# Kernel tuning notes

Measured on AMD Instinct MI355X. Metric: run time of the kernel, lower is better.

The kernel has to match this reference:

```python
import jax, jax.numpy as jnp
import numpy as np

N_HEADS = 8
ATT_DIM = 64


def _pos_enc(x):
    # x: (chan, L, bs, D); sinusoidal PE added along axis -3 (the query/key slot dim)
    L, D = x.shape[-3], x.shape[-1]
    pos = np.arange(L)[:, None].astype(np.float32)
    div = np.exp(np.arange(0, D, 2).astype(np.float32) * (-np.log(10000.0) / D))
    pe = np.zeros((L, 1, D), dtype=np.float32)
    pe[:, 0, 0::2] = np.sin(pos * div)
    pe[:, 0, 1::2] = np.cos(pos * div)
    return x + jnp.asarray(pe)


def setup_inputs() -> dict:
    key = jax.random.key(0)
    ks = jax.random.split(key, 6)
    C, NQ, NK, B, QD, KD = 8, 16, 32, 128, 128, 128
    E = N_HEADS * ATT_DIM  # 512
    OUT = ATT_DIM  # out_dim defaults to attention_dim
    b = np.float32(1.0 / np.sqrt(ATT_DIM))
    bp = np.float32(1.0 / np.sqrt(OUT))
    return {
        "q": jax.random.normal(ks[0], (C, NQ, B, QD), dtype=jnp.float32),
        "k": jax.random.normal(ks[1], (C, NK, B, KD), dtype=jnp.float32),
        "Wq": jax.random.uniform(ks[2], (C, NQ, QD, E), jnp.float32, -b, b),
        "Wk": jax.random.uniform(ks[3], (C, NK, KD, E), jnp.float32, -b, b),
        "Wv": jax.random.uniform(ks[4], (C, NK, KD, E), jnp.float32, -b, b),
        "Wp": jax.random.uniform(ks[5], (C, NQ, E, OUT), jnp.float32, -bp, bp),
    }


def reference(q, k, Wq, Wk, Wv, Wp):
    H, A = N_HEADS, ATT_DIM
    C, NQ, B, _ = q.shape
    NK = k.shape[1]
    inv_temp = jnp.float32(1.0 / np.sqrt(A))
    q_pe = _pos_enc(q)
    k_pe = _pos_enc(k)
    # per-channel grouped QKV projections: (C, N, B, D) x (C, N, D, E) -> (C, N, B, E)
    query = jnp.einsum('cqbd,cqde->cqbe', q_pe, Wq).reshape(C, NQ, B, H, A)
    key_t = jnp.einsum('ckbd,ckde->ckbe', k_pe, Wk).reshape(C, NK, B, H, A)
    value = jnp.einsum('ckbd,ckde->ckbe', k_pe, Wv).reshape(C, NK, B, H, A)
    # attention scores per (channel, batch, head)
    logits = jnp.einsum('cqbha,ckbha->cbhqk', query, key_t) * inv_temp
    attn = jax.nn.softmax(logits, axis=-1)
    # value aggregation (original does broadcast-multiply+sum; einsum is the same math)
    out = jnp.einsum('cbhqk,ckbha->cqbha', attn, value).reshape(C, NQ, B, H * A)
    # per-channel output projection
    return jnp.einsum('cqbe,cqeo->cqbo', out, Wp)
```

## Files before the change

kernel.cpp:

```cpp
#include <hip/hip_runtime.h>

#define C_  8
#define NQ_ 16
#define NK_ 32
#define B_  128
#define D_  128
#define E_  512
#define H_  8
#define A_  64
#define O_  64

typedef __attribute__((ext_vector_type(4))) float f32x4;
typedef __attribute__((ext_vector_type(8))) short bf16x8;
typedef __attribute__((ext_vector_type(4))) short bf16x4;

__device__ __forceinline__ short f2bf(float f) {
    union { float f; unsigned u; } v; v.f = f;
    unsigned r = v.u + 0x7fffu + ((v.u >> 16) & 1u);
    return (short)(r >> 16);
}

__global__ __launch_bounds__(256) void qkv_proj_kernel(
    const float* __restrict__ qin, const float* __restrict__ kin,
    const float* __restrict__ Wq, const float* __restrict__ Wk,
    const float* __restrict__ Wv,
    short* __restrict__ wsq, short* __restrict__ wsk, short* __restrict__ wsv)
{
    __shared__ __align__(16) short Alds[B_][72];
    __shared__ __align__(16) short Blds[128][72];
    __shared__ float pe_buf[D_];

    const int tid   = threadIdx.x;
    const int blk   = blockIdx.x;
    const int e_blk = blk & 3;
    const int unit  = blk >> 2;

    const float* X; const float* W; short* Y; int n;
    if (unit < C_ * NQ_) {
        n = unit % NQ_;
        X = qin + (size_t)unit * B_ * D_;
        W = Wq  + (size_t)unit * D_ * E_;
        Y = wsq + (size_t)unit * B_ * E_;
    } else if (unit < C_ * (NQ_ + NK_)) {
        const int u = unit - C_ * NQ_;
        n = u % NK_;
        X = kin + (size_t)u * B_ * D_;
        W = Wk  + (size_t)u * D_ * E_;
        Y = wsk + (size_t)u * B_ * E_;
    } else {
        const int u = unit - C_ * (NQ_ + NK_);
        n = u % NK_;
        X = kin + (size_t)u * B_ * D_;
        W = Wv  + (size_t)u * D_ * E_;
        Y = wsv + (size_t)u * B_ * E_;
    }

    if (tid < D_) {
        const int d = tid;
        const float freq = expf((float)(d & ~1) * (-9.210340371976184f / (float)D_));
        const float arg  = (float)n * freq;
        pe_buf[d] = (d & 1) ? cosf(arg) : sinf(arg);
    }
    __syncthreads();

    const int wv   = tid >> 6;
    const int lane = tid & 63;
    const int lr   = lane & 15;
    const int quad = lane >> 4;
    const int wrow = (wv >> 1) * 64;
    const int wcol = (wv & 1) * 64;

    f32x4 acc[4][4];
    for (int m = 0; m < 4; ++m)
        for (int nf = 0; nf < 4; ++nf)
            acc[m][nf] = (f32x4){0.f, 0.f, 0.f, 0.f};

    const int e  = tid & 127;
    const int kg = (tid >> 7) * 32;

    for (int k0 = 0; k0 < D_; k0 += 64) {
        f32x4 a_raw[8];
        #pragma unroll
        for (int i = 0; i < 8; ++i) {
            const int id  = tid + 256 * i;
            const int row = id >> 4;
            const int ch  = id & 15;
            a_raw[i] = *(const f32x4*)(X + (size_t)row * D_ + k0 + ch * 4);
        }
        float b_raw[32];
        const float* bsrc = W + (size_t)(k0 + kg) * E_ + e_blk * 128 + e;
        #pragma unroll
        for (int i = 0; i < 32; ++i)
            b_raw[i] = bsrc[(size_t)i * E_];

        #pragma unroll
        for (int i = 0; i < 8; ++i) {
            const int id  = tid + 256 * i;
            const int row = id >> 4;
            const int ch  = id & 15;
            bf16x4 v;
            #pragma unroll
            for (int j = 0; j < 4; ++j)
                v[j] = f2bf(a_raw[i][j] + pe_buf[k0 + ch * 4 + j]);
            *(bf16x4*)&Alds[row][ch * 4] = v;
        }
        #pragma unroll
        for (int i = 0; i < 4; ++i) {
            bf16x8 v;
            #pragma unroll
            for (int j = 0; j < 8; ++j)
                v[j] = f2bf(b_raw[i * 8 + j]);
            *(bf16x8*)&Blds[e][kg + i * 8] = v;
        }
        __syncthreads();

        for (int ks = 0; ks < 2; ++ks) {
            const int kc = ks * 32 + quad * 8;
            bf16x8 af[4], bfr[4];
            for (int m = 0; m < 4; ++m)
                af[m] = *(const bf16x8*)&Alds[wrow + m * 16 + lr][kc];
            for (int nf = 0; nf < 4; ++nf)
                bfr[nf] = *(const bf16x8*)&Blds[wcol + nf * 16 + lr][kc];
            for (int m = 0; m < 4; ++m)
                for (int nf = 0; nf < 4; ++nf)
                    acc[m][nf] = __builtin_amdgcn_mfma_f32_16x16x32_bf16(
                        af[m], bfr[nf], acc[m][nf], 0, 0, 0);
        }
        __syncthreads();
    }

    for (int m = 0; m < 4; ++m)
        for (int nf = 0; nf < 4; ++nf)
            for (int r = 0; r < 4; ++r) {
                const int row = wrow + m * 16 + quad * 4 + r;
                const int col = e_blk * 128 + wcol + nf * 16 + lr;
                Y[(size_t)row * E_ + col] = f2bf(acc[m][nf][r]);
            }
}

__global__ __launch_bounds__(256) void attn_kernel(
    const short* __restrict__ wsq, const short* __restrict__ wsk,
    const short* __restrict__ wsv, short* __restrict__ wso)
{
    __shared__ __align__(16) short Qs[16][264];
    __shared__ __align__(16) short Ks[32][264];
    __shared__ __align__(16) short Vs[32][258];
    __shared__ __align__(16) short Ps[4][16][40];

    const int tid = threadIdx.x;
    const int blk = blockIdx.x;
    const int hh  = blk & 1;
    const int b   = (blk >> 1) & (B_ - 1);
    const int c   = blk >> 8;

    const size_t rowstride = (size_t)B_ * E_;
    const size_t ebase = (size_t)b * E_ + hh * 256;

    {
        const int nloc = tid >> 5;
        const int bi   = tid & 31;
        const short* qb = wsq + (size_t)c * NQ_ * rowstride + ebase + bi * 8;
        const short* kb = wsk + (size_t)c * NK_ * rowstride + ebase + bi * 8;
        const short* vb = wsv + (size_t)c * NK_ * rowstride + ebase + bi * 8;
        #pragma unroll
        for (int i = 0; i < 2; ++i) {
            const int nn = nloc + i * 8;
            *(bf16x8*)&Qs[nn][bi * 8] = *(const bf16x8*)(qb + (size_t)nn * rowstride);
        }
        #pragma unroll
        for (int i = 0; i < 4; ++i) {
            const int nn = nloc + i * 8;
            *(bf16x8*)&Ks[nn][bi * 8] = *(const bf16x8*)(kb + (size_t)nn * rowstride);
        }
        #pragma unroll
        for (int i = 0; i < 4; ++i) {
            const int nn = nloc + i * 8;
            bf16x8 v = *(const bf16x8*)(vb + (size_t)nn * rowstride);
            #pragma unroll
            for (int p = 0; p < 4; ++p)
                *(int*)&Vs[nn][bi * 8 + p * 2] = ((const int*)&v)[p];
        }
    }
    __syncthreads();

    const int wv   = tid >> 6;
    const int lane = tid & 63;
    const int lr   = lane & 15;
    const int quad = lane >> 4;
    const int lcol = wv * 64;

    f32x4 sacc0 = (f32x4){0.f, 0.f, 0.f, 0.f};
    f32x4 sacc1 = (f32x4){0.f, 0.f, 0.f, 0.f};
    #pragma unroll
    for (int ks = 0; ks < 2; ++ks) {
        const int kc = lcol + ks * 32 + quad * 8;
        const bf16x8 aq  = *(const bf16x8*)&Qs[lr][kc];
        const bf16x8 bk0 = *(const bf16x8*)&Ks[lr][kc];
        const bf16x8 bk1 = *(const bf16x8*)&Ks[16 + lr][kc];
        sacc0 = __builtin_amdgcn_mfma_f32_16x16x32_bf16(aq, bk0, sacc0, 0, 0, 0);
        sacc1 = __builtin_amdgcn_mfma_f32_16x16x32_bf16(aq, bk1, sacc1, 0, 0, 0);
    }

    float p0[4], p1[4];
    for (int r = 0; r < 4; ++r) {
        const float v0 = sacc0[r] * 0.125f;
        const float v1 = sacc1[r] * 0.125f;
        float m = fmaxf(v0, v1);
        m = fmaxf(m, __shfl_xor(m, 1));
        m = fmaxf(m, __shfl_xor(m, 2));
        m = fmaxf(m, __shfl_xor(m, 4));
        m = fmaxf(m, __shfl_xor(m, 8));
        const float e0 = __expf(v0 - m);
        const float e1 = __expf(v1 - m);
        float s = e0 + e1;
        s += __shfl_xor(s, 1);
        s += __shfl_xor(s, 2);
        s += __shfl_xor(s, 4);
        s += __shfl_xor(s, 8);
        const float inv = 1.0f / s;
        p0[r] = e0 * inv;
        p1[r] = e1 * inv;
    }

    for (int r = 0; r < 4; ++r) {
        Ps[wv][quad * 4 + r][lr]      = f2bf(p0[r]);
        Ps[wv][quad * 4 + r][16 + lr] = f2bf(p1[r]);
    }
    __syncthreads();
    const bf16x8 ap = *(const bf16x8*)&Ps[wv][lr][quad * 8];

    #pragma unroll
    for (int t = 0; t < 4; ++t) {
        bf16x8 bvv;
        #pragma unroll
        for (int j = 0; j < 8; ++j)
            bvv[j] = Vs[quad * 8 + j][lcol + t * 16 + lr];
        f32x4 oacc = (f32x4){0.f, 0.f, 0.f, 0.f};
        oacc = __builtin_amdgcn_mfma_f32_16x16x32_bf16(ap, bvv, oacc, 0, 0, 0);
        for (int r = 0; r < 4; ++r)
            wso[((size_t)(c * NQ_ + quad * 4 + r) * B_ + b) * E_
                + hh * 256 + lcol + t * 16 + lr] = f2bf(oacc[r]);
    }
}

__global__ __launch_bounds__(256) void out_proj_kernel(
    const short* __restrict__ wso, const float* __restrict__ Wp,
    float* __restrict__ out)
{
    __shared__ __align__(16) short Xlds[64][72];
    __shared__ __align__(16) short Wlds[64][72];

    const int tid  = threadIdx.x;
    const int blk  = blockIdx.x;
    const int cq   = blk >> 1;
    const int half = blk & 1;

    const short* Xb = wso + (size_t)cq * B_ * E_ + (size_t)half * 64 * E_;
    const float* Wb = Wp  + (size_t)cq * E_ * O_;
    float*       Ob = out + (size_t)cq * B_ * O_ + (size_t)half * 64 * O_;

    const int wv   = tid >> 6;
    const int lane = tid & 63;
    const int lr   = lane & 15;
    const int quad = lane >> 4;

    f32x4 acc[4];
    for (int nf = 0; nf < 4; ++nf) acc[nf] = (f32x4){0.f, 0.f, 0.f, 0.f};

    const int o   = tid & 63;
    const int grp = tid >> 6;

    for (int k0 = 0; k0 < E_; k0 += 64) {
        bf16x8 xv[2];
        #pragma unroll
        for (int i = 0; i < 2; ++i) {
            const int task = tid + 256 * i;
            const int row  = task >> 3;
            const int oct  = task & 7;
            xv[i] = *(const bf16x8*)(Xb + (size_t)row * E_ + k0 + oct * 8);
        }
        float wr[16];
        #pragma unroll
        for (int j = 0; j < 16; ++j)
            wr[j] = Wb[(size_t)(k0 + grp * 16 + j) * O_ + o];

        #pragma unroll
        for (int i = 0; i < 2; ++i) {
            const int task = tid + 256 * i;
            const int row  = task >> 3;
            const int oct  = task & 7;
            *(bf16x8*)&Xlds[row][oct * 8] = xv[i];
        }
        bf16x8 w0, w1;
        #pragma unroll
        for (int j = 0; j < 8; ++j) { w0[j] = f2bf(wr[j]); w1[j] = f2bf(wr[8 + j]); }
        *(bf16x8*)&Wlds[o][grp * 16]     = w0;
        *(bf16x8*)&Wlds[o][grp * 16 + 8] = w1;
        __syncthreads();

        for (int ks = 0; ks < 2; ++ks) {
            const int kc = ks * 32 + quad * 8;
            const bf16x8 af = *(const bf16x8*)&Xlds[wv * 16 + lr][kc];
            for (int nf = 0; nf < 4; ++nf) {
                const bf16x8 bfr = *(const bf16x8*)&Wlds[nf * 16 + lr][kc];
                acc[nf] = __builtin_amdgcn_mfma_f32_16x16x32_bf16(af, bfr, acc[nf], 0, 0, 0);
            }
        }
        __syncthreads();
    }

    for (int nf = 0; nf < 4; ++nf)
        for (int r = 0; r < 4; ++r)
            Ob[(size_t)(wv * 16 + quad * 4 + r) * O_ + nf * 16 + lr] = acc[nf][r];
}

extern "C" void kernel_launch(void* const* d_in, const int* in_sizes, int n_in,
                              void* d_out, int out_size, void* d_ws, size_t ws_size,
                              hipStream_t stream) {
    const float* q  = (const float*)d_in[0];
    const float* k  = (const float*)d_in[1];
    const float* Wq = (const float*)d_in[2];
    const float* Wk = (const float*)d_in[3];
    const float* Wv = (const float*)d_in[4];
    const float* Wp = (const float*)d_in[5];
    float* out = (float*)d_out;

    const size_t sz_q = (size_t)C_ * NQ_ * B_ * E_;
    const size_t sz_k = (size_t)C_ * NK_ * B_ * E_;
    short* wsq = (short*)d_ws;
    short* wsk = wsq + sz_q;
    short* wsv = wsk + sz_k;
    short* wso = wsv + sz_k;

    qkv_proj_kernel<<<dim3(2560), dim3(256), 0, stream>>>(q, k, Wq, Wk, Wv, wsq, wsk, wsv);
    attn_kernel<<<dim3(2048), dim3(256), 0, stream>>>(wsq, wsk, wsv, wso);
    out_proj_kernel<<<dim3(256), dim3(256), 0, stream>>>(wso, Wp, out);
}
```

Before: 248.2 us.

## Store QKV workspace batch-major; split out-projection over output halves with prefetch

The QKV projection now writes its bf16 results in a (c, b, n, e) layout, so each attention block reads contiguous rows for its batch element instead of rows strided by B*E. The output projection grid is doubled by splitting the 64 output columns into two halves, and global loads for the next K-step are issued before the current step's LDS store and MFMA work. The projection's writes become strided across n in exchange for contiguous attention reads. The out-projection split re-reads the X tile twice in exchange for more blocks.

```diff
diff --git a/kernel.cpp b/kernel.cpp
--- a/kernel.cpp
+++ b/kernel.cpp
@@ -35,24 +35,30 @@
     const int e_blk = blk & 3;
     const int unit  = blk >> 2;
 
-    const float* X; const float* W; short* Y; int n;
+    const float* X; const float* W; short* Y; int n; size_t ypitch;
     if (unit < C_ * NQ_) {
-        n = unit % NQ_;
+        const int c = unit >> 4;
+        n = unit & 15;
         X = qin + (size_t)unit * B_ * D_;
         W = Wq  + (size_t)unit * D_ * E_;
-        Y = wsq + (size_t)unit * B_ * E_;
+        Y = wsq + (size_t)c * B_ * NQ_ * E_ + (size_t)n * E_;
+        ypitch = (size_t)NQ_ * E_;
     } else if (unit < C_ * (NQ_ + NK_)) {
         const int u = unit - C_ * NQ_;
-        n = u % NK_;
+        const int c = u >> 5;
+        n = u & 31;
         X = kin + (size_t)u * B_ * D_;
         W = Wk  + (size_t)u * D_ * E_;
-        Y = wsk + (size_t)u * B_ * E_;
+        Y = wsk + (size_t)c * B_ * NK_ * E_ + (size_t)n * E_;
+        ypitch = (size_t)NK_ * E_;
     } else {
         const int u = unit - C_ * (NQ_ + NK_);
-        n = u % NK_;
+        const int c = u >> 5;
+        n = u & 31;
         X = kin + (size_t)u * B_ * D_;
         W = Wv  + (size_t)u * D_ * E_;
-        Y = wsv + (size_t)u * B_ * E_;
+        Y = wsv + (size_t)c * B_ * NK_ * E_ + (size_t)n * E_;
+        ypitch = (size_t)NK_ * E_;
     }
 
     if (tid < D_) {
@@ -134,7 +140,7 @@
             for (int r = 0; r < 4; ++r) {
                 const int row = wrow + m * 16 + quad * 4 + r;
                 const int col = e_blk * 128 + wcol + nf * 16 + lr;
-                Y[(size_t)row * E_ + col] = f2bf(acc[m][nf][r]);
+                Y[(size_t)row * ypitch + col] = f2bf(acc[m][nf][r]);
             }
 }
 
@@ -153,32 +159,30 @@
     const int b   = (blk >> 1) & (B_ - 1);
     const int c   = blk >> 8;
 
-    const size_t rowstride = (size_t)B_ * E_;
-    const size_t ebase = (size_t)b * E_ + hh * 256;
+    const short* qb = wsq + ((size_t)(c * B_ + b) * NQ_) * E_ + hh * 256;
+    const short* kb = wsk + ((size_t)(c * B_ + b) * NK_) * E_ + hh * 256;
+    const short* vb = wsv + ((size_t)(c * B_ + b) * NK_) * E_ + hh * 256;
 
     {
         const int nloc = tid >> 5;
-        const int bi   = tid & 31;
-        const short* qb = wsq + (size_t)c * NQ_ * rowstride + ebase + bi * 8;
-        const short* kb = wsk + (size_t)c * NK_ * rowstride + ebase + bi * 8;
-        const short* vb = wsv + (size_t)c * NK_ * rowstride + ebase + bi * 8;
+        const int ch   = tid & 31;
         #pragma unroll
         for (int i = 0; i < 2; ++i) {
             const int nn = nloc + i * 8;
-            *(bf16x8*)&Qs[nn][bi * 8] = *(const bf16x8*)(qb + (size_t)nn * rowstride);
+            *(bf16x8*)&Qs[nn][ch * 8] = *(const bf16x8*)(qb + (size_t)nn * E_ + ch * 8);
         }
         #pragma unroll
         for (int i = 0; i < 4; ++i) {
             const int nn = nloc + i * 8;
-            *(bf16x8*)&Ks[nn][bi * 8] = *(const bf16x8*)(kb + (size_t)nn * rowstride);
+            *(bf16x8*)&Ks[nn][ch * 8] = *(const bf16x8*)(kb + (size_t)nn * E_ + ch * 8);
         }
         #pragma unroll
         for (int i = 0; i < 4; ++i) {
             const int nn = nloc + i * 8;
-            bf16x8 v = *(const bf16x8*)(vb + (size_t)nn * rowstride);
+            bf16x8 v = *(const bf16x8*)(vb + (size_t)nn * E_ + ch * 8);
             #pragma unroll
             for (int p = 0; p < 4; ++p)
-                *(int*)&Vs[nn][bi * 8 + p * 2] = ((const int*)&v)[p];
+                *(int*)&Vs[nn][ch * 8 + p * 2] = ((const int*)&v)[p];
         }
     }
     __syncthreads();
@@ -248,60 +252,67 @@
     float* __restrict__ out)
 {
     __shared__ __align__(16) short Xlds[64][72];
-    __shared__ __align__(16) short Wlds[64][72];
-
-    const int tid  = threadIdx.x;
-    const int blk  = blockIdx.x;
-    const int cq   = blk >> 1;
-    const int half = blk & 1;
-
-    const short* Xb = wso + (size_t)cq * B_ * E_ + (size_t)half * 64 * E_;
-    const float* Wb = Wp  + (size_t)cq * E_ * O_;
-    float*       Ob = out + (size_t)cq * B_ * O_ + (size_t)half * 64 * O_;
+    __shared__ __align__(16) short Wlds[32][72];
+
+    const int tid = threadIdx.x;
+    const int blk = blockIdx.x;
+    const int cq  = blk >> 2;
+    const int bh  = (blk >> 1) & 1;
+    const int oh  = blk & 1;
+
+    const short* Xb = wso + (size_t)cq * B_ * E_ + (size_t)bh * 64 * E_;
+    const float* Wb = Wp  + (size_t)cq * E_ * O_ + oh * 32;
+    float*       Ob = out + (size_t)cq * B_ * O_ + (size_t)bh * 64 * O_ + oh * 32;
 
     const int wv   = tid >> 6;
     const int lane = tid & 63;
     const int lr   = lane & 15;
     const int quad = lane >> 4;
-
-    f32x4 acc[4];
-    for (int nf = 0; nf < 4; ++nf) acc[nf] = (f32x4){0.f, 0.f, 0.f, 0.f};
-
-    const int o   = tid & 63;
-    const int grp = tid >> 6;
-
-    for (int k0 = 0; k0 < E_; k0 += 64) {
-        bf16x8 xv[2];
+    const int o    = tid & 31;
+    const int kg   = tid >> 5;
+
+    f32x4 acc[2];
+    acc[0] = (f32x4){0.f, 0.f, 0.f, 0.f};
+    acc[1] = (f32x4){0.f, 0.f, 0.f, 0.f};
+
+    bf16x8 xv[2][2];
+    float  wr[2][8];
+
+    auto issue = [&](int s, int buf) {
+        const int k0 = s * 64;
         #pragma unroll
         for (int i = 0; i < 2; ++i) {
             const int task = tid + 256 * i;
-            const int row  = task >> 3;
-            const int oct  = task & 7;
-            xv[i] = *(const bf16x8*)(Xb + (size_t)row * E_ + k0 + oct * 8);
-        }
-        float wr[16];
-        #pragma unroll
-        for (int j = 0; j < 16; ++j)
-            wr[j] = Wb[(size_t)(k0 + grp * 16 + j) * O_ + o];
+            xv[buf][i] = *(const bf16x8*)(Xb + (size_t)(task >> 3) * E_ + k0 + (task & 7) * 8);
+        }
+        #pragma unroll
+        for (int j = 0; j < 8; ++j)
+            wr[buf][j] = Wb[(size_t)(k0 + kg * 8 + j) * O_ + o];
+    };
+
+    issue(0, 0);
+    #pragma unroll
+    for (int s = 0; s < 8; ++s) {
+        const int cb = s & 1;
+        if (s < 7) issue(s + 1, cb ^ 1);
 
         #pragma unroll
         for (int i = 0; i < 2; ++i) {
             const int task = tid + 256 * i;
-            const int row  = task >> 3;
-            const int oct  = task & 7;
-            *(bf16x8*)&Xlds[row][oct * 8] = xv[i];
-        }
-        bf16x8 w0, w1;
-        #pragma unroll
-        for (int j = 0; j < 8; ++j) { w0[j] = f2bf(wr[j]); w1[j] = f2bf(wr[8 + j]); }
-        *(bf16x8*)&Wlds[o][grp * 16]     = w0;
-        *(bf16x8*)&Wlds[o][grp * 16 + 8] = w1;
+            *(bf16x8*)&Xlds[task >> 3][(task & 7) * 8] = xv[cb][i];
+        }
+        bf16x8 wv8;
+        #pragma unroll
+        for (int j = 0; j < 8; ++j) wv8[j] = f2bf(wr[cb][j]);
+        *(bf16x8*)&Wlds[o][kg * 8] = wv8;
         __syncthreads();
 
+        #pragma unroll
         for (int ks = 0; ks < 2; ++ks) {
             const int kc = ks * 32 + quad * 8;
             const bf16x8 af = *(const bf16x8*)&Xlds[wv * 16 + lr][kc];
-            for (int nf = 0; nf < 4; ++nf) {
+            #pragma unroll
+            for (int nf = 0; nf < 2; ++nf) {
                 const bf16x8 bfr = *(const bf16x8*)&Wlds[nf * 16 + lr][kc];
                 acc[nf] = __builtin_amdgcn_mfma_f32_16x16x32_bf16(af, bfr, acc[nf], 0, 0, 0);
             }
@@ -309,7 +320,8 @@
         __syncthreads();
     }
 
-    for (int nf = 0; nf < 4; ++nf)
+    #pragma unroll
+    for (int nf = 0; nf < 2; ++nf)
         for (int r = 0; r < 4; ++r)
             Ob[(size_t)(wv * 16 + quad * 4 + r) * O_ + nf * 16 + lr] = acc[nf][r];
 }
@@ -334,5 +346,5 @@
 
     qkv_proj_kernel<<<dim3(2560), dim3(256), 0, stream>>>(q, k, Wq, Wk, Wv, wsq, wsk, wsv);
     attn_kernel<<<dim3(2048), dim3(256), 0, stream>>>(wsq, wsk, wsv, wso);
-    out_proj_kernel<<<dim3(256), dim3(256), 0, stream>>>(wso, Wp, out);
-}
+    out_proj_kernel<<<dim3(512), dim3(256), 0, stream>>>(wso, Wp, out);
+}
```

After: 246.7 us. About the same (-0.6%).
